# Kernel tuning notes

Measured on AMD Instinct MI355X. Metric: run time of the kernel, lower is better.

Reference implementation:

```python
import math
import jax, jax.numpy as jnp
import numpy as np

B, T, C, H = 2, 1024, 1024, 16
D = C // H
NEG = -jnp.inf


def setup_inputs() -> dict:
    key = jax.random.key(0)
    ks = jax.random.split(key, 4)
    x_star = jax.random.normal(ks[0], (B, T, C), jnp.float32)
    x_hat = jax.random.normal(ks[1], (B, T, C), jnp.float32)
    # attn_masks semantics: True = keep. star-keys: causal; hat-keys: diagonal only.
    keep_star = jnp.broadcast_to(jnp.tril(jnp.ones((T, T), bool)), (B, T, T))
    keep_hat = jnp.broadcast_to(jnp.eye(T, dtype=bool), (B, T, T))
    W_attn = jax.random.normal(ks[2], (C, 3 * C), jnp.float32) * (1.0 / math.sqrt(C))
    b_attn = jnp.zeros((3 * C,), jnp.float32)
    W_proj = jax.random.normal(ks[3], (C, C), jnp.float32) * (1.0 / math.sqrt(C))
    b_proj = jnp.zeros((C,), jnp.float32)
    return dict(x_star=x_star, x_hat=x_hat, keep_star=keep_star, keep_hat=keep_hat,
                W_attn=W_attn, b_attn=b_attn, W_proj=W_proj, b_proj=b_proj)


def _interleave(x_star, x_hat, keep_star, keep_hat, W_attn, b_attn, W_proj, b_proj):
    def qkv(x):
        q, k, v = jnp.split(x @ W_attn + b_attn, 3, axis=-1)
        r = lambda t: t.reshape(B, T, H, D).transpose(0, 2, 1, 3)  # (B,H,T,D)
        return r(q), r(k), r(v)

    q_s, k_s, v_s = qkv(x_star)
    q_h, k_h, v_h = qkv(x_hat)

    scale = 1.0 / math.sqrt(D)
    attend = lambda q, k: jnp.einsum('bhqd,bhkd->bhqk', q, k) * scale

    # blocking masks (True = block), broadcast over heads
    mask_star = ~keep_star[:, None, :, :]
    mask_hat = ~keep_hat[:, None, :, :]
    mask_causal = ~jnp.tril(jnp.ones((T, T), bool))[None, None]

    def mlp(y):  # (B,H,T,D) -> (B,T,C)
        y = y.transpose(0, 2, 1, 3).reshape(B, T, C)
        return y @ W_proj + b_proj  # resid_dropout is identity in eval

    # star stream: plain causal self-attention
    att_star = jnp.where(mask_causal, NEG, attend(q_s, k_s))
    y_star = mlp(jax.nn.softmax(att_star, axis=-1) @ v_s)

    # hat stream: merge two score streams (hat queries vs star keys / hat keys)
    att_hs = jnp.where(mask_star, NEG, attend(q_h, k_s))
    att_hh = jnp.where(mask_hat, NEG, attend(q_h, k_h))
    merged = jnp.where(jnp.isinf(att_hh), att_hs, att_hh)
    p = jax.nn.softmax(merged, axis=-1)
    y_hat = (jnp.where(mask_star, 0.0, p) @ v_s
             + jnp.where(mask_hat, 0.0, p) @ v_h)
    y_hat = mlp(y_hat)
    return y_star, y_hat


def reference(x_star, x_hat, keep_star, keep_hat, W_attn, b_attn, W_proj, b_proj):
    return _interleave(x_star, x_hat, keep_star, keep_hat, W_attn, b_attn, W_proj, b_proj)
```

## Files before the change

kernel.cpp:

```cpp
#include <hip/hip_runtime.h>
#include <math.h>

#define T_ 1024
#define C_ 1024
#define H_ 16
#define D_ 64
#define B_ 2
#define M2 (B_*T_*C_)
#define SCALE 0.125f

typedef __attribute__((ext_vector_type(8))) short bf16x8;
typedef __attribute__((ext_vector_type(8))) unsigned short ushort8;
typedef __attribute__((ext_vector_type(4))) float f32x4;

__device__ inline unsigned short f2bf(float f) {
  unsigned int u = __float_as_uint(f);
  u += 0x7fff + ((u >> 16) & 1);
  return (unsigned short)(u >> 16);
}
__device__ inline float bf2f(unsigned short u) {
  return __uint_as_float(((unsigned int)u) << 16);
}

__device__ inline void load16(unsigned short* lds, const unsigned short* g) {
  __builtin_amdgcn_global_load_lds(
      (const __attribute__((address_space(1))) unsigned int*)g,
      (__attribute__((address_space(3))) unsigned int*)lds, 16, 0, 0);
}

__global__ __launch_bounds__(256) void convert_x(
    const float* __restrict__ xs, const float* __restrict__ xh,
    unsigned short* __restrict__ Xbf)
{
  size_t c = (size_t)blockIdx.x * 256 + threadIdx.x;
  size_t e = c * 4;
  const float* src = (e < (size_t)2048 * 1024) ? (xs + e)
                                               : (xh + e - (size_t)2048 * 1024);
  float4 v = *(const float4*)src;
  ushort4 o;
  o.x = f2bf(v.x); o.y = f2bf(v.y); o.z = f2bf(v.z); o.w = f2bf(v.w);
  *(ushort4*)(Xbf + e) = o;
}

__global__ __launch_bounds__(256) void transpose_w(
    const float* __restrict__ Win, unsigned short* __restrict__ Wout, int N)
{
  __shared__ float Ts[64][65];
  const int n0 = blockIdx.x * 64, k0 = blockIdx.y * 64;
  const int tid = threadIdx.x;
#pragma unroll
  for (int p = 0; p < 4; ++p) {
    int chunk = tid + p * 256;
    int r = chunk >> 4, c4 = chunk & 15;
    float4 v = *(const float4*)(Win + (size_t)(k0 + r) * N + n0 + c4 * 4);
    Ts[r][c4*4+0] = v.x; Ts[r][c4*4+1] = v.y;
    Ts[r][c4*4+2] = v.z; Ts[r][c4*4+3] = v.w;
  }
  __syncthreads();
#pragma unroll
  for (int p = 0; p < 2; ++p) {
    int chunk = tid + p * 256;
    int n = chunk >> 3, kq = chunk & 7;
    ushort8 o;
#pragma unroll
    for (int j = 0; j < 8; ++j) o[j] = f2bf(Ts[kq * 8 + j][n]);
    *(ushort8*)(Wout + (size_t)(n0 + n) * 1024 + k0 + kq * 8) = o;
  }
}

#define GEMM_MAIN_LOOP(Aptr, Bptr)                                             \
  for (int k0 = 0; k0 < 1024; k0 += 64) {                                      \
    __syncthreads();                                                           \
    _Pragma("unroll")                                                          \
    for (int it = 0; it < 4; ++it) {                                           \
      int chunk = tid + it * 256;                                              \
      int row = chunk >> 3, cq = chunk & 7;                                    \
      int gq = cq ^ (row & 7);                                                 \
      load16(As + chunk * 8, Aptr + (size_t)(row0 + row) * 1024 + k0 + gq*8);  \
      load16(Bs + chunk * 8, Bptr + (size_t)(col0 + row) * 1024 + k0 + gq*8);  \
    }                                                                          \
    __syncthreads();                                                           \
    _Pragma("unroll")                                                          \
    for (int kb = 0; kb < 2; ++kb) {                                           \
      bf16x8 af[4], bfr[4];                                                    \
      int q = kb * 4 + quad;                                                   \
      _Pragma("unroll")                                                        \
      for (int mt = 0; mt < 4; ++mt) {                                         \
        int m = wm * 64 + mt * 16 + lane16;                                    \
        af[mt] = *(const bf16x8*)&As[m * 64 + (q ^ (m & 7)) * 8];              \
      }                                                                        \
      _Pragma("unroll")                                                        \
      for (int nt = 0; nt < 4; ++nt) {                                         \
        int n = wn * 64 + nt * 16 + lane16;                                    \
        bfr[nt] = *(const bf16x8*)&Bs[n * 64 + (q ^ (n & 7)) * 8];             \
      }                                                                        \
      _Pragma("unroll")                                                        \
      for (int mt = 0; mt < 4; ++mt)                                           \
        _Pragma("unroll")                                                      \
        for (int nt = 0; nt < 4; ++nt)                                         \
          acc[mt][nt] = __builtin_amdgcn_mfma_f32_16x16x32_bf16(               \
              af[mt], bfr[nt], acc[mt][nt], 0, 0, 0);                          \
    }                                                                          \
  }

__global__ __launch_bounds__(256) void qkv_mfma(
    const unsigned short* __restrict__ A,
    const unsigned short* __restrict__ Bt,
    const float* __restrict__ bias,
    unsigned short* __restrict__ qkv)
{
  __shared__ __align__(16) unsigned short As[128 * 64];
  __shared__ __align__(16) unsigned short Bs[128 * 64];
  const int tid = threadIdx.x;
  const int col0 = blockIdx.x * 128;
  const int row0 = blockIdx.y * 128;
  const int w = tid >> 6, lane = tid & 63;
  const int lane16 = lane & 15, quad = lane >> 4;
  const int wm = w >> 1, wn = w & 1;
  f32x4 acc[4][4];
#pragma unroll
  for (int mt = 0; mt < 4; ++mt)
#pragma unroll
    for (int nt = 0; nt < 4; ++nt) acc[mt][nt] = (f32x4){0.f, 0.f, 0.f, 0.f};

  GEMM_MAIN_LOOP(A, Bt)

#pragma unroll
  for (int mt = 0; mt < 4; ++mt) {
#pragma unroll
    for (int nt = 0; nt < 4; ++nt) {
      int gn = col0 + wn * 64 + nt * 16 + lane16;
      int which = gn >> 10, c = gn & 1023;
      int h = c >> 6, d = c & 63;
      float bv = bias[gn];
#pragma unroll
      for (int r = 0; r < 4; ++r) {
        int gm = row0 + wm * 64 + mt * 16 + quad * 4 + r;
        int s = gm >> 11, b = (gm >> 10) & 1, t = gm & 1023;
        qkv[(size_t)(s * 3 + which) * M2 +
            ((size_t)(b * 16 + h) * 1024 + t) * 64 + d] =
            f2bf(acc[mt][nt][r] + bv);
      }
    }
  }
}

__global__ __launch_bounds__(256) void proj_mfma(
    const unsigned short* __restrict__ A,
    const unsigned short* __restrict__ Bt,
    const float* __restrict__ bias,
    float* __restrict__ out)
{
  __shared__ __align__(16) unsigned short As[128 * 64];
  __shared__ __align__(16) unsigned short Bs[128 * 64];
  const int tid = threadIdx.x;
  const int col0 = blockIdx.x * 128;
  const int row0 = blockIdx.y * 128;
  const int w = tid >> 6, lane = tid & 63;
  const int lane16 = lane & 15, quad = lane >> 4;
  const int wm = w >> 1, wn = w & 1;
  f32x4 acc[4][4];
#pragma unroll
  for (int mt = 0; mt < 4; ++mt)
#pragma unroll
    for (int nt = 0; nt < 4; ++nt) acc[mt][nt] = (f32x4){0.f, 0.f, 0.f, 0.f};

  GEMM_MAIN_LOOP(A, Bt)

#pragma unroll
  for (int mt = 0; mt < 4; ++mt) {
#pragma unroll
    for (int nt = 0; nt < 4; ++nt) {
      int gn = col0 + wn * 64 + nt * 16 + lane16;
      float bv = bias[gn];
#pragma unroll
      for (int r = 0; r < 4; ++r) {
        int gm = row0 + wm * 64 + mt * 16 + quad * 4 + r;
        out[(size_t)gm * 1024 + gn] = acc[mt][nt][r] + bv;
      }
    }
  }
}

__global__ __launch_bounds__(256) void attn_kernel(
    const unsigned short* __restrict__ ws, unsigned short* __restrict__ Y)
{
  __shared__ __align__(16) unsigned short Qs[64][72];
  __shared__ __align__(16) unsigned short Ks[64][72];
  __shared__ __align__(16) unsigned short Vt[64][72];
  __shared__ __align__(16) unsigned short Ps[4][16][72];
  __shared__ float diag[64];

  const int tid = threadIdx.x;
  const int bx  = blockIdx.x;
  const int p   = bx & 7;
  const int h   = (bx >> 3) & 15;
  const int b   = (bx >> 7) & 1;
  const int s   = (bx >> 8) & 1;
  const size_t hb = (size_t)(b * H_ + h) * T_ * D_;

  const unsigned short* Qg  = ws + (size_t)(s ? 3 : 0) * M2 + hb;
  const unsigned short* Kg  = ws + (size_t)1 * M2 + hb;
  const unsigned short* Vg  = ws + (size_t)2 * M2 + hb;
  const unsigned short* Khg = ws + (size_t)4 * M2 + hb;
  const unsigned short* Vhg = ws + (size_t)5 * M2 + hb;

  const int w = tid >> 6, lane = tid & 63;
  const int lane16 = lane & 15, quad = lane >> 4;
  const int wq0 = w * 16;

  for (int tt = 0; tt < 2; ++tt) {
    const int qt = tt ? (15 - p) : p;
    const int i0 = qt * 64;

    __syncthreads();
    for (int idx = tid; idx < 512; idx += 256) {
      int row = idx >> 3, ch = idx & 7;
      *(ushort8*)&Qs[row][ch * 8] =
          *(const ushort8*)(Qg + (size_t)(i0 + row) * 64 + ch * 8);
    }
    __syncthreads();
    if (s == 1 && tid < 64) {
      const unsigned short* kh = Khg + (size_t)(i0 + tid) * 64;
      float sum = 0.f;
#pragma unroll 8
      for (int d = 0; d < 64; ++d) sum += bf2f(Qs[tid][d]) * bf2f(kh[d]);
      diag[tid] = sum * SCALE;
    }
    bf16x8 qf[2];
    qf[0] = *(const bf16x8*)&Qs[wq0 + lane16][quad * 8];
    qf[1] = *(const bf16x8*)&Qs[wq0 + lane16][32 + quad * 8];

    float mrun[4], lrun[4];
    f32x4 O[4];
#pragma unroll
    for (int r2 = 0; r2 < 4; ++r2) {
      mrun[r2] = -INFINITY; lrun[r2] = 0.f;
      O[r2] = (f32x4){0.f, 0.f, 0.f, 0.f};
    }

    for (int kt = 0; kt <= qt; ++kt) {
      __syncthreads();
      for (int idx = tid; idx < 512; idx += 256) {
        int row = idx >> 3, ch = idx & 7;
        *(ushort8*)&Ks[row][ch * 8] =
            *(const ushort8*)(Kg + (size_t)(kt * 64 + row) * 64 + ch * 8);
        ushort8 v = *(const ushort8*)(Vg + (size_t)(kt * 64 + row) * 64 + ch * 8);
#pragma unroll
        for (int j = 0; j < 8; ++j) Vt[ch * 8 + j][row] = v[j];
      }
      __syncthreads();

      f32x4 S[4];
#pragma unroll
      for (int nt = 0; nt < 4; ++nt) S[nt] = (f32x4){0.f, 0.f, 0.f, 0.f};
#pragma unroll
      for (int kb = 0; kb < 2; ++kb) {
#pragma unroll
        for (int nt = 0; nt < 4; ++nt) {
          bf16x8 bk = *(const bf16x8*)&Ks[nt * 16 + lane16][kb * 32 + quad * 8];
          S[nt] = __builtin_amdgcn_mfma_f32_16x16x32_bf16(qf[kb], bk, S[nt], 0, 0, 0);
        }
      }

      float mt4[4] = {-INFINITY, -INFINITY, -INFINITY, -INFINITY};
#pragma unroll
      for (int nt = 0; nt < 4; ++nt) {
        int gj = kt * 64 + nt * 16 + lane16;
#pragma unroll
        for (int r = 0; r < 4; ++r) {
          int gi = i0 + wq0 + quad * 4 + r;
          float v = S[nt][r] * SCALE;
          if (gj > gi) v = -INFINITY;
          if (s == 1 && kt == qt && gj == gi) v = diag[wq0 + quad * 4 + r];
          S[nt][r] = v;
          mt4[r] = fmaxf(mt4[r], v);
        }
      }
#pragma unroll
      for (int m = 1; m < 16; m <<= 1)
#pragma unroll
        for (int r = 0; r < 4; ++r)
          mt4[r] = fmaxf(mt4[r], __shfl_xor(mt4[r], m, 64));
      float alpha[4], rsum[4];
#pragma unroll
      for (int r = 0; r < 4; ++r) {
        float mnew = fmaxf(mrun[r], mt4[r]);
        alpha[r] = __expf(mrun[r] - mnew);
        mrun[r] = mnew;
        rsum[r] = 0.f;
      }
#pragma unroll
      for (int nt = 0; nt < 4; ++nt)
#pragma unroll
        for (int r = 0; r < 4; ++r) {
          float pv = __expf(S[nt][r] - mrun[r]);
          S[nt][r] = pv;
          rsum[r] += pv;
        }
#pragma unroll
      for (int m = 1; m < 16; m <<= 1)
#pragma unroll
        for (int r = 0; r < 4; ++r)
          rsum[r] += __shfl_xor(rsum[r], m, 64);
#pragma unroll
      for (int r = 0; r < 4; ++r) {
        lrun[r] = lrun[r] * alpha[r] + rsum[r];
#pragma unroll
        for (int nt = 0; nt < 4; ++nt) O[nt][r] *= alpha[r];
      }

#pragma unroll
      for (int nt = 0; nt < 4; ++nt)
#pragma unroll
        for (int r = 0; r < 4; ++r)
          Ps[w][quad * 4 + r][nt * 16 + lane16] = f2bf(S[nt][r]);

#pragma unroll
      for (int kb = 0; kb < 2; ++kb) {
        bf16x8 pa = *(const bf16x8*)&Ps[w][lane16][kb * 32 + quad * 8];
#pragma unroll
        for (int nt = 0; nt < 4; ++nt) {
          bf16x8 vb = *(const bf16x8*)&Vt[nt * 16 + lane16][kb * 32 + quad * 8];
          O[nt] = __builtin_amdgcn_mfma_f32_16x16x32_bf16(pa, vb, O[nt], 0, 0, 0);
        }
      }

      if (s == 1 && kt == qt) {
#pragma unroll
        for (int r = 0; r < 4; ++r) {
          float pd = __expf(diag[wq0 + quad * 4 + r] - mrun[r]);
          const unsigned short* vh = Vhg + (size_t)(i0 + wq0 + quad * 4 + r) * 64;
#pragma unroll
          for (int nt = 0; nt < 4; ++nt)
            O[nt][r] += pd * bf2f(vh[nt * 16 + lane16]);
        }
      }
    }

#pragma unroll
    for (int r = 0; r < 4; ++r) {
      int gi = i0 + wq0 + quad * 4 + r;
      float linv = 1.f / lrun[r];
      unsigned short* yo = Y + ((size_t)(s * 2048 + b * 1024 + gi)) * 1024 + h * 64;
#pragma unroll
      for (int nt = 0; nt < 4; ++nt)
        yo[nt * 16 + lane16] = f2bf(O[nt][r] * linv);
    }
  }
}

extern "C" void kernel_launch(void* const* d_in, const int* in_sizes, int n_in,
                              void* d_out, int out_size, void* d_ws, size_t ws_size,
                              hipStream_t stream) {
  (void)in_sizes; (void)n_in; (void)out_size; (void)ws_size;
  const float* xs = (const float*)d_in[0];
  const float* xh = (const float*)d_in[1];
  const float* Wa = (const float*)d_in[4];
  const float* ba = (const float*)d_in[5];
  const float* Wp = (const float*)d_in[6];
  const float* bp = (const float*)d_in[7];

  unsigned short* qkv = (unsigned short*)d_ws;
  unsigned short* Ybf = qkv + (size_t)6 * M2;
  unsigned short* Xbf = Ybf + (size_t)4 * 1024 * 1024;
  unsigned short* WaT = Xbf + (size_t)4 * 1024 * 1024;
  unsigned short* WpT = WaT + (size_t)3 * 1024 * 1024;
  float* out = (float*)d_out;

  convert_x  <<<4096, 256, 0, stream>>>(xs, xh, Xbf);
  transpose_w<<<dim3(48, 16), 256, 0, stream>>>(Wa, WaT, 3072);
  transpose_w<<<dim3(16, 16), 256, 0, stream>>>(Wp, WpT, 1024);
  qkv_mfma   <<<dim3(24, 32), 256, 0, stream>>>(Xbf, WaT, ba, qkv);
  attn_kernel<<<dim3(512), 256, 0, stream>>>(qkv, Ybf);
  proj_mfma  <<<dim3(8, 32), 256, 0, stream>>>(Ybf, WpT, bp, out);
}
```

Measured before the change: 222.6 us.

## Rework attention kernel with double-buffered async loads, swizzled LDS, and exp2 softmax

Rewrites the attention kernel so each block handles one query tile, launching 1024 blocks ordered longest-first instead of pairing tiles. K and a pre-transposed V are prefetched with double-buffered global_load_lds into XOR-swizzled LDS, which removes the per-iteration scalar transpose and one barrier. Scores are computed transposed (K as the A operand) so each lane holds one query row, which simplifies the max/sum reductions to two shuffles. The QKV GEMM epilogue folds scale*log2e into Q and writes star-V transposed so softmax can use exp2 directly. This trades extra epilogue index logic and more blocks for less LDS transpose work and better load/compute overlap.

```diff
diff --git a/kernel.cpp b/kernel.cpp
--- a/kernel.cpp
+++ b/kernel.cpp
@@ -7,11 +7,15 @@
 #define D_ 64
 #define B_ 2
 #define M2 (B_*T_*C_)
-#define SCALE 0.125f
+#define QSC 0.18033688f
 
 typedef __attribute__((ext_vector_type(8))) short bf16x8;
 typedef __attribute__((ext_vector_type(8))) unsigned short ushort8;
 typedef __attribute__((ext_vector_type(4))) float f32x4;
+
+__device__ inline float fast_exp2(float x) {
+  return __builtin_amdgcn_exp2f(x);
+}
 
 __device__ inline unsigned short f2bf(float f) {
   unsigned int u = __float_as_uint(f);
@@ -20,6 +24,13 @@
 }
 __device__ inline float bf2f(unsigned short u) {
   return __uint_as_float(((unsigned int)u) << 16);
+}
+__device__ inline unsigned int pack2bf(float lo, float hi) {
+  unsigned int ul = __float_as_uint(lo);
+  unsigned int uh = __float_as_uint(hi);
+  ul += 0x7fff + ((ul >> 16) & 1);
+  uh += 0x7fff + ((uh >> 16) & 1);
+  return (ul >> 16) | (uh & 0xffff0000u);
 }
 
 __device__ inline void load16(unsigned short* lds, const unsigned short* g) {
@@ -137,9 +148,15 @@
       for (int r = 0; r < 4; ++r) {
         int gm = row0 + wm * 64 + mt * 16 + quad * 4 + r;
         int s = gm >> 11, b = (gm >> 10) & 1, t = gm & 1023;
-        qkv[(size_t)(s * 3 + which) * M2 +
-            ((size_t)(b * 16 + h) * 1024 + t) * 64 + d] =
-            f2bf(acc[mt][nt][r] + bv);
+        float val = acc[mt][nt][r] + bv;
+        if (which == 0) val *= QSC;
+        size_t idx;
+        if (which == 2 && s == 0)
+          idx = (size_t)2 * M2 + ((size_t)(b * 16 + h) * 64 + d) * 1024 + t;
+        else
+          idx = (size_t)(s * 3 + which) * M2 +
+                ((size_t)(b * 16 + h) * 1024 + t) * 64 + d;
+        qkv[idx] = f2bf(val);
       }
     }
   }
@@ -185,168 +202,189 @@
 __global__ __launch_bounds__(256) void attn_kernel(
     const unsigned short* __restrict__ ws, unsigned short* __restrict__ Y)
 {
-  __shared__ __align__(16) unsigned short Qs[64][72];
-  __shared__ __align__(16) unsigned short Ks[64][72];
-  __shared__ __align__(16) unsigned short Vt[64][72];
+  __shared__ __align__(16) unsigned short Qs[64 * 64];
+  __shared__ __align__(16) unsigned short Ks[2][64 * 64];
+  __shared__ __align__(16) unsigned short Vts[2][64 * 64];
   __shared__ __align__(16) unsigned short Ps[4][16][72];
   __shared__ float diag[64];
 
   const int tid = threadIdx.x;
   const int bx  = blockIdx.x;
-  const int p   = bx & 7;
-  const int h   = (bx >> 3) & 15;
-  const int b   = (bx >> 7) & 1;
-  const int s   = (bx >> 8) & 1;
+  const int inner = bx & 63;
+  const int h = inner & 15;
+  const int b = (inner >> 4) & 1;
+  const int s = (inner >> 5) & 1;
+  const int qt = 15 - (bx >> 6);
+  const int i0 = qt * 64;
   const size_t hb = (size_t)(b * H_ + h) * T_ * D_;
 
   const unsigned short* Qg  = ws + (size_t)(s ? 3 : 0) * M2 + hb;
   const unsigned short* Kg  = ws + (size_t)1 * M2 + hb;
-  const unsigned short* Vg  = ws + (size_t)2 * M2 + hb;
+  const unsigned short* VTg = ws + (size_t)2 * M2 + hb;
   const unsigned short* Khg = ws + (size_t)4 * M2 + hb;
   const unsigned short* Vhg = ws + (size_t)5 * M2 + hb;
 
-  const int w = tid >> 6, lane = tid & 63;
+  const int lane = tid & 63;
+  const int w = tid >> 6;
   const int lane16 = lane & 15, quad = lane >> 4;
   const int wq0 = w * 16;
 
-  for (int tt = 0; tt < 2; ++tt) {
-    const int qt = tt ? (15 - p) : p;
-    const int i0 = qt * 64;
-
-    __syncthreads();
-    for (int idx = tid; idx < 512; idx += 256) {
-      int row = idx >> 3, ch = idx & 7;
-      *(ushort8*)&Qs[row][ch * 8] =
-          *(const ushort8*)(Qg + (size_t)(i0 + row) * 64 + ch * 8);
-    }
-    __syncthreads();
-    if (s == 1 && tid < 64) {
+#pragma unroll
+  for (int it = 0; it < 2; ++it) {
+    int ch = tid + it * 256;
+    int row = ch >> 3, cq = ch & 7, gq = cq ^ (row & 7);
+    load16(Qs + ch * 8, Qg + (size_t)(i0 + row) * 64 + gq * 8);
+    load16(&Ks[0][ch * 8], Kg + (size_t)(0 * 64 + row) * 64 + gq * 8);
+    load16(&Vts[0][ch * 8], VTg + (size_t)row * 1024 + 0 * 64 + gq * 8);
+  }
+  __syncthreads();
+
+  bf16x8 qf[2];
+  {
+    int m = wq0 + lane16;
+    qf[0] = *(const bf16x8*)&Qs[m * 64 + ((quad) ^ (m & 7)) * 8];
+    qf[1] = *(const bf16x8*)&Qs[m * 64 + ((4 + quad) ^ (m & 7)) * 8];
+  }
+  if (s == 1) {
+    if (tid < 64) {
       const unsigned short* kh = Khg + (size_t)(i0 + tid) * 64;
       float sum = 0.f;
-#pragma unroll 8
-      for (int d = 0; d < 64; ++d) sum += bf2f(Qs[tid][d]) * bf2f(kh[d]);
-      diag[tid] = sum * SCALE;
-    }
-    bf16x8 qf[2];
-    qf[0] = *(const bf16x8*)&Qs[wq0 + lane16][quad * 8];
-    qf[1] = *(const bf16x8*)&Qs[wq0 + lane16][32 + quad * 8];
-
-    float mrun[4], lrun[4];
-    f32x4 O[4];
-#pragma unroll
-    for (int r2 = 0; r2 < 4; ++r2) {
-      mrun[r2] = -INFINITY; lrun[r2] = 0.f;
-      O[r2] = (f32x4){0.f, 0.f, 0.f, 0.f};
-    }
-
-    for (int kt = 0; kt <= qt; ++kt) {
-      __syncthreads();
-      for (int idx = tid; idx < 512; idx += 256) {
-        int row = idx >> 3, ch = idx & 7;
-        *(ushort8*)&Ks[row][ch * 8] =
-            *(const ushort8*)(Kg + (size_t)(kt * 64 + row) * 64 + ch * 8);
-        ushort8 v = *(const ushort8*)(Vg + (size_t)(kt * 64 + row) * 64 + ch * 8);
-#pragma unroll
-        for (int j = 0; j < 8; ++j) Vt[ch * 8 + j][row] = v[j];
-      }
-      __syncthreads();
-
-      f32x4 S[4];
-#pragma unroll
-      for (int nt = 0; nt < 4; ++nt) S[nt] = (f32x4){0.f, 0.f, 0.f, 0.f};
-#pragma unroll
-      for (int kb = 0; kb < 2; ++kb) {
-#pragma unroll
-        for (int nt = 0; nt < 4; ++nt) {
-          bf16x8 bk = *(const bf16x8*)&Ks[nt * 16 + lane16][kb * 32 + quad * 8];
-          S[nt] = __builtin_amdgcn_mfma_f32_16x16x32_bf16(qf[kb], bk, S[nt], 0, 0, 0);
+#pragma unroll
+      for (int c = 0; c < 8; ++c) {
+        bf16x8 qv = *(const bf16x8*)&Qs[tid * 64 + (c ^ (tid & 7)) * 8];
+        ushort8 kv = *(const ushort8*)(kh + c * 8);
+#pragma unroll
+        for (int j = 0; j < 8; ++j)
+          sum += bf2f((unsigned short)qv[j]) * bf2f(kv[j]);
+      }
+      diag[tid] = sum;
+    }
+    __syncthreads();
+  }
+
+  float mrun = -INFINITY, lrun = 0.f;
+  f32x4 O[4];
+#pragma unroll
+  for (int nt = 0; nt < 4; ++nt) O[nt] = (f32x4){0.f, 0.f, 0.f, 0.f};
+
+  for (int kt = 0; kt <= qt; ++kt) {
+    const int cur = kt & 1;
+    if (kt < qt) {
+      const int nxt = 1 - cur;
+#pragma unroll
+      for (int it = 0; it < 2; ++it) {
+        int ch = tid + it * 256;
+        int row = ch >> 3, cq = ch & 7, gq = cq ^ (row & 7);
+        load16(&Ks[nxt][ch * 8], Kg + (size_t)((kt + 1) * 64 + row) * 64 + gq * 8);
+        load16(&Vts[nxt][ch * 8], VTg + (size_t)row * 1024 + (kt + 1) * 64 + gq * 8);
+      }
+    }
+
+    f32x4 St[4];
+#pragma unroll
+    for (int mt = 0; mt < 4; ++mt) St[mt] = (f32x4){0.f, 0.f, 0.f, 0.f};
+#pragma unroll
+    for (int kb = 0; kb < 2; ++kb) {
+#pragma unroll
+      for (int mt = 0; mt < 4; ++mt) {
+        int m = mt * 16 + lane16;
+        bf16x8 kf = *(const bf16x8*)&Ks[cur][m * 64 + ((kb * 4 + quad) ^ (m & 7)) * 8];
+        St[mt] = __builtin_amdgcn_mfma_f32_16x16x32_bf16(kf, qf[kb], St[mt], 0, 0, 0);
+      }
+    }
+
+    if (kt == qt) {
+      const int kstar = wq0 + lane16;
+      const float dv = (s == 1) ? diag[kstar] : 0.f;
+#pragma unroll
+      for (int mt = 0; mt < 4; ++mt)
+#pragma unroll
+        for (int r = 0; r < 4; ++r) {
+          int key = mt * 16 + quad * 4 + r;
+          float v = St[mt][r];
+          if (s == 1 && key == kstar) v = dv;
+          if (key > kstar) v = -INFINITY;
+          St[mt][r] = v;
         }
-      }
-
-      float mt4[4] = {-INFINITY, -INFINITY, -INFINITY, -INFINITY};
+    }
+
+    float mt_ = -INFINITY;
+#pragma unroll
+    for (int mt = 0; mt < 4; ++mt)
+#pragma unroll
+      for (int r = 0; r < 4; ++r) mt_ = fmaxf(mt_, St[mt][r]);
+    mt_ = fmaxf(mt_, __shfl_xor(mt_, 16, 64));
+    mt_ = fmaxf(mt_, __shfl_xor(mt_, 32, 64));
+    float mnew = fmaxf(mrun, mt_);
+    float alpha = fast_exp2(mrun - mnew);
+    mrun = mnew;
+    float rsum = 0.f;
+#pragma unroll
+    for (int mt = 0; mt < 4; ++mt)
+#pragma unroll
+      for (int r = 0; r < 4; ++r) {
+        float p = fast_exp2(St[mt][r] - mnew);
+        St[mt][r] = p;
+        rsum += p;
+      }
+    rsum += __shfl_xor(rsum, 16, 64);
+    rsum += __shfl_xor(rsum, 32, 64);
+    lrun = lrun * alpha + rsum;
+
+#pragma unroll
+    for (int mt = 0; mt < 4; ++mt) {
+      *(unsigned int*)&Ps[w][lane16][mt * 16 + quad * 4] =
+          pack2bf(St[mt][0], St[mt][1]);
+      *(unsigned int*)&Ps[w][lane16][mt * 16 + quad * 4 + 2] =
+          pack2bf(St[mt][2], St[mt][3]);
+    }
+
+    float a4[4];
+#pragma unroll
+    for (int r = 0; r < 4; ++r) a4[r] = __shfl(alpha, quad * 4 + r, 16);
+#pragma unroll
+    for (int nt = 0; nt < 4; ++nt)
+#pragma unroll
+      for (int r = 0; r < 4; ++r) O[nt][r] *= a4[r];
+
+#pragma unroll
+    for (int kb = 0; kb < 2; ++kb) {
+      bf16x8 pa = *(const bf16x8*)&Ps[w][lane16][kb * 32 + quad * 8];
 #pragma unroll
       for (int nt = 0; nt < 4; ++nt) {
-        int gj = kt * 64 + nt * 16 + lane16;
-#pragma unroll
-        for (int r = 0; r < 4; ++r) {
-          int gi = i0 + wq0 + quad * 4 + r;
-          float v = S[nt][r] * SCALE;
-          if (gj > gi) v = -INFINITY;
-          if (s == 1 && kt == qt && gj == gi) v = diag[wq0 + quad * 4 + r];
-          S[nt][r] = v;
-          mt4[r] = fmaxf(mt4[r], v);
-        }
-      }
-#pragma unroll
-      for (int m = 1; m < 16; m <<= 1)
-#pragma unroll
-        for (int r = 0; r < 4; ++r)
-          mt4[r] = fmaxf(mt4[r], __shfl_xor(mt4[r], m, 64));
-      float alpha[4], rsum[4];
+        int n = nt * 16 + lane16;
+        bf16x8 vb = *(const bf16x8*)&Vts[cur][n * 64 + ((kb * 4 + quad) ^ (n & 7)) * 8];
+        O[nt] = __builtin_amdgcn_mfma_f32_16x16x32_bf16(pa, vb, O[nt], 0, 0, 0);
+      }
+    }
+
+    if (s == 1 && kt == qt) {
+      float pd = fast_exp2(diag[wq0 + lane16] - mrun);
+      float p4[4];
+#pragma unroll
+      for (int r = 0; r < 4; ++r) p4[r] = __shfl(pd, quad * 4 + r, 16);
 #pragma unroll
       for (int r = 0; r < 4; ++r) {
-        float mnew = fmaxf(mrun[r], mt4[r]);
-        alpha[r] = __expf(mrun[r] - mnew);
-        mrun[r] = mnew;
-        rsum[r] = 0.f;
-      }
-#pragma unroll
-      for (int nt = 0; nt < 4; ++nt)
-#pragma unroll
-        for (int r = 0; r < 4; ++r) {
-          float pv = __expf(S[nt][r] - mrun[r]);
-          S[nt][r] = pv;
-          rsum[r] += pv;
-        }
-#pragma unroll
-      for (int m = 1; m < 16; m <<= 1)
-#pragma unroll
-        for (int r = 0; r < 4; ++r)
-          rsum[r] += __shfl_xor(rsum[r], m, 64);
-#pragma unroll
-      for (int r = 0; r < 4; ++r) {
-        lrun[r] = lrun[r] * alpha[r] + rsum[r];
-#pragma unroll
-        for (int nt = 0; nt < 4; ++nt) O[nt][r] *= alpha[r];
-      }
-
-#pragma unroll
-      for (int nt = 0; nt < 4; ++nt)
-#pragma unroll
-        for (int r = 0; r < 4; ++r)
-          Ps[w][quad * 4 + r][nt * 16 + lane16] = f2bf(S[nt][r]);
-
-#pragma unroll
-      for (int kb = 0; kb < 2; ++kb) {
-        bf16x8 pa = *(const bf16x8*)&Ps[w][lane16][kb * 32 + quad * 8];
-#pragma unroll
-        for (int nt = 0; nt < 4; ++nt) {
-          bf16x8 vb = *(const bf16x8*)&Vt[nt * 16 + lane16][kb * 32 + quad * 8];
-          O[nt] = __builtin_amdgcn_mfma_f32_16x16x32_bf16(pa, vb, O[nt], 0, 0, 0);
-        }
-      }
-
-      if (s == 1 && kt == qt) {
-#pragma unroll
-        for (int r = 0; r < 4; ++r) {
-          float pd = __expf(diag[wq0 + quad * 4 + r] - mrun[r]);
-          const unsigned short* vh = Vhg + (size_t)(i0 + wq0 + quad * 4 + r) * 64;
-#pragma unroll
-          for (int nt = 0; nt < 4; ++nt)
-            O[nt][r] += pd * bf2f(vh[nt * 16 + lane16]);
-        }
-      }
-    }
-
-#pragma unroll
-    for (int r = 0; r < 4; ++r) {
-      int gi = i0 + wq0 + quad * 4 + r;
-      float linv = 1.f / lrun[r];
-      unsigned short* yo = Y + ((size_t)(s * 2048 + b * 1024 + gi)) * 1024 + h * 64;
-#pragma unroll
-      for (int nt = 0; nt < 4; ++nt)
-        yo[nt * 16 + lane16] = f2bf(O[nt][r] * linv);
-    }
+        const unsigned short* vh = Vhg + (size_t)(i0 + wq0 + quad * 4 + r) * 64;
+#pragma unroll
+        for (int nt = 0; nt < 4; ++nt)
+          O[nt][r] += p4[r] * bf2f(vh[nt * 16 + lane16]);
+      }
+    }
+    __syncthreads();
+  }
+
+  float l4[4];
+#pragma unroll
+  for (int r = 0; r < 4; ++r) l4[r] = __shfl(lrun, quad * 4 + r, 16);
+#pragma unroll
+  for (int r = 0; r < 4; ++r) {
+    int gi = i0 + wq0 + quad * 4 + r;
+    float inv = 1.f / l4[r];
+    unsigned short* yo = Y + ((size_t)(s * 2048 + b * 1024 + gi)) * 1024 + h * 64;
+#pragma unroll
+    for (int nt = 0; nt < 4; ++nt)
+      yo[nt * 16 + lane16] = f2bf(O[nt][r] * inv);
   }
 }
 
@@ -372,6 +410,6 @@
   transpose_w<<<dim3(48, 16), 256, 0, stream>>>(Wa, WaT, 3072);
   transpose_w<<<dim3(16, 16), 256, 0, stream>>>(Wp, WpT, 1024);
   qkv_mfma   <<<dim3(24, 32), 256, 0, stream>>>(Xbf, WaT, ba, qkv);
-  attn_kernel<<<dim3(512), 256, 0, stream>>>(qkv, Ybf);
+  attn_kernel<<<dim3(1024), 256, 0, stream>>>(qkv, Ybf);
   proj_mfma  <<<dim3(8, 32), 256, 0, stream>>>(Ybf, WpT, bp, out);
 }
```

After: 194.2 us. 12.8% less time.
